# Kernel tuning notes

Measured on AMD Instinct MI355X. Metric: run time of the kernel, lower is better.

Reference implementation:

```python
import jax, jax.numpy as jnp
import numpy as np

N_NODES = 100000
N_EDGES = 1600000
D = 64


def setup_inputs() -> dict:
    key = jax.random.key(0)
    ks = jax.random.split(key, 9)
    x = jax.random.normal(ks[0], (N_NODES, D), dtype=jnp.float32)
    edge_index = jax.random.randint(ks[1], (2, N_EDGES), 0, N_NODES, dtype=jnp.int64)
    W_self = jax.random.normal(ks[2], (D, D), dtype=jnp.float32) * (D ** -0.5)
    b_self = jax.random.normal(ks[3], (D,), dtype=jnp.float32) * 0.01
    W_neigh = jax.random.normal(ks[4], (D, D), dtype=jnp.float32) * (D ** -0.5)
    b_neigh = jax.random.normal(ks[5], (D,), dtype=jnp.float32) * 0.01
    W_var = jax.random.normal(ks[6], (D, D), dtype=jnp.float32) * (D ** -0.5)
    b_var = jax.random.normal(ks[7], (D,), dtype=jnp.float32) * 0.01
    return {"x": x, "edge_index": edge_index, "W_self": W_self, "b_self": b_self,
            "W_neigh": W_neigh, "b_neigh": b_neigh, "W_var": W_var, "b_var": b_var}


def reference(x, edge_index, W_self, b_self, W_neigh, b_neigh, W_var, b_var):
    N, d = x.shape
    scale = d ** -0.5
    src, dst = edge_index[0], edge_index[1]

    x_src = x[src]                                   # [E, d]
    x_dst = x[dst]                                   # [E, d]

    # reciprocal attention: scatter_softmax over incoming edges of dst
    logits = jnp.sum(x_src * x_dst, axis=-1) * scale               # [E]
    seg_max = jax.ops.segment_max(logits, dst, num_segments=N)     # [N]
    ex = jnp.exp(logits - seg_max[dst])                            # [E]
    denom = jax.ops.segment_sum(ex, dst, num_segments=N)           # [N]
    attn = ex / denom[dst]                                         # [E]

    msg = jax.ops.segment_sum(x_src * attn[:, None], dst, num_segments=N)  # [N, d]

    out = x @ W_self.T + b_self + msg @ W_neigh.T + b_neigh

    # variance via double scatter_mean
    cnt = jax.ops.segment_sum(jnp.ones_like(logits), dst, num_segments=N)
    cnt = jnp.maximum(cnt, 1.0)[:, None]                           # [N, 1]
    msg_mean = jax.ops.segment_sum(x_src, dst, num_segments=N) / cnt
    diff_sq = (x_src - msg_mean[dst]) ** 2                         # [E, d]
    var = jax.ops.segment_sum(diff_sq, dst, num_segments=N) / cnt  # [N, d]

    out = out + var @ W_var.T + b_var
    return out
```

## Files before the change

kernel.cpp:

```cpp
#include <hip/hip_runtime.h>


static inline size_t ws_align(size_t x) { return (x + 255) & ~size_t(255); }

typedef __attribute__((ext_vector_type(8))) short bf16x8;
typedef __attribute__((ext_vector_type(4))) float f32x4;
typedef __attribute__((ext_vector_type(2))) float f32x2;

#define ECHUNK 2048

__device__ __forceinline__ unsigned short f2bf(float f) {
    unsigned u = __builtin_bit_cast(unsigned, f);
    u += 0x7FFFu + ((u >> 16) & 1u);
    return (unsigned short)(u >> 16);
}
__device__ __forceinline__ float bfhi(int d) {
    return __builtin_bit_cast(float, (unsigned)d & 0xFFFF0000u);
}
__device__ __forceinline__ float bflo(int d) {
    return __builtin_bit_cast(float, (unsigned)d << 16);
}

template <int CTRL>
__device__ __forceinline__ float dpp_radd(float t) {
    int v = __builtin_amdgcn_update_dpp(0, __builtin_bit_cast(int, t),
                                        CTRL, 0xF, 0xF, true);
    return t + __builtin_bit_cast(float, v);
}
__device__ __forceinline__ float row16_sum(float t) {
    t = dpp_radd<0xB1>(t);
    t = dpp_radd<0x4E>(t);
    t = dpp_radd<0x124>(t);
    t = dpp_radd<0x128>(t);
    return t;
}

__global__ void __launch_bounds__(256) hist_cast_kernel(
        const float* __restrict__ x, unsigned short* __restrict__ xb,
        const int* __restrict__ ei, int* __restrict__ hist,
        int E, int n4, int nblk, int nb1) {
    __shared__ int h[512];
    for (int k = threadIdx.x; k < nb1; k += 256) h[k] = 0;
    int stride = gridDim.x * 256;
    for (int i = blockIdx.x * 256 + threadIdx.x; i < n4; i += stride) {
        float4 v = ((const float4*)x)[i];
        ushort4 hh; hh.x = f2bf(v.x); hh.y = f2bf(v.y); hh.z = f2bf(v.z); hh.w = f2bf(v.w);
        ((ushort4*)xb)[i] = hh;
    }
    __syncthreads();
    const int* dstp = ei + E;
    int base = blockIdx.x * ECHUNK;
    #pragma unroll 4
    for (int k = 0; k < ECHUNK / 256; ++k) {
        int e = base + k * 256 + threadIdx.x;
        if (e < E) atomicAdd(&h[dstp[e] >> 8], 1);
    }
    __syncthreads();
    for (int k = threadIdx.x; k < nb1; k += 256) hist[k * nblk + blockIdx.x] = h[k];
}

__global__ void scan_a_kernel(int* __restrict__ h, int* __restrict__ bsum, int M) {
    __shared__ int t[256];
    int i = blockIdx.x * 256 + threadIdx.x;
    int v = (i < M) ? h[i] : 0;
    t[threadIdx.x] = v;
    __syncthreads();
    for (int off = 1; off < 256; off <<= 1) {
        int u = (threadIdx.x >= (unsigned)off) ? t[threadIdx.x - off] : 0;
        __syncthreads();
        t[threadIdx.x] += u;
        __syncthreads();
    }
    if (i < M) h[i] = t[threadIdx.x] - v;
    if (threadIdx.x == 255) bsum[blockIdx.x] = t[255];
}

__global__ void scan_b_kernel(int* __restrict__ bsum, int nb) {
    __shared__ int t[1024];
    __shared__ int carry;
    if (threadIdx.x == 0) carry = 0;
    __syncthreads();
    for (int base = 0; base < nb; base += 1024) {
        int i = base + threadIdx.x;
        int v = (i < nb) ? bsum[i] : 0;
        t[threadIdx.x] = v;
        __syncthreads();
        for (int off = 1; off < 1024; off <<= 1) {
            int u = (threadIdx.x >= off) ? t[threadIdx.x - off] : 0;
            __syncthreads();
            t[threadIdx.x] += u;
            __syncthreads();
        }
        int c = carry;
        if (i < nb) bsum[i] = t[threadIdx.x] - v + c;
        __syncthreads();
        if (threadIdx.x == 1023) carry = c + t[1023];
        __syncthreads();
    }
}

__global__ void __launch_bounds__(256) part_kernel(
        const int* __restrict__ ei, const int* __restrict__ offs,
        const int* __restrict__ bsum, int* __restrict__ tmp,
        int E, int nblk, int nb1) {
    __shared__ int lofs[512];
    int b = blockIdx.x;
    for (int k = threadIdx.x; k < nb1; k += 256) {
        int idx = k * nblk + b;
        lofs[k] = offs[idx] + bsum[idx >> 8];
    }
    __syncthreads();
    const int* dstp = ei + E;
    int base = b * ECHUNK;
    #pragma unroll 4
    for (int k = 0; k < ECHUNK / 256; ++k) {
        int e = base + k * 256 + threadIdx.x;
        if (e < E) {
            int dst = dstp[e];
            int src = ei[e];
            int pos = atomicAdd(&lofs[dst >> 8], 1);
            tmp[pos] = (src << 8) | (dst & 255);
        }
    }
}

__global__ void __launch_bounds__(256) fsort_kernel(
        const int* __restrict__ tmp, const int* __restrict__ offs,
        const int* __restrict__ bsum, int* __restrict__ srcs,
        int* __restrict__ rs, int E, int N, int nblk, int nb1) {
    __shared__ int cnt[256], sc[256], lofs[256];
    int b = blockIdx.x, tid = threadIdx.x;
    int i0 = b * nblk;
    int start = offs[i0] + bsum[i0 >> 8];
    int end;
    if (b == nb1 - 1) end = E;
    else { int i1 = (b + 1) * nblk; end = offs[i1] + bsum[i1 >> 8]; }

    cnt[tid] = 0;
    __syncthreads();
    for (int e = start + tid; e < end; e += 256) atomicAdd(&cnt[tmp[e] & 255], 1);
    __syncthreads();
    int c = cnt[tid];
    sc[tid] = c;
    __syncthreads();
    for (int off = 1; off < 256; off <<= 1) {
        int u = (tid >= off) ? sc[tid - off] : 0;
        __syncthreads();
        sc[tid] += u;
        __syncthreads();
    }
    int excl = sc[tid] - c;
    int node = b * 256 + tid;
    if (node < N) rs[node] = start + excl;
    lofs[tid] = start + excl;
    __syncthreads();
    for (int e = start + tid; e < end; e += 256) {
        int v = tmp[e];
        int pos = atomicAdd(&lofs[v & 255], 1);
        srcs[pos] = v >> 8;
    }
    if (b == 0 && tid == 0) rs[N] = E;
}

__global__ void __launch_bounds__(256) node_gather_kernel(
        const unsigned short* __restrict__ xb,
        const int* __restrict__ rs, const int* __restrict__ srcs,
        unsigned short* __restrict__ msgvar, int N) {
    int w = (blockIdx.x * blockDim.x + threadIdx.x) >> 6;
    if (w >= N) return;
    int lane = threadIdx.x & 63;
    int q = lane & 15;
    int g = lane >> 4;
    int s = rs[w], e = rs[w + 1];
    const int2* xb2 = (const int2*)xb;
    int2 dn = xb2[(size_t)w * 16 + q];
    f32x2 xn01 = {bflo(dn.x), bfhi(dn.x)}, xn23 = {bflo(dn.y), bfhi(dn.y)};
    float den = 0.f;
    f32x2 sxa = {0,0}, sxb = {0,0}, ssqa = {0,0}, ssqb = {0,0},
          smea = {0,0}, smeb = {0,0};

    auto compute = [&](int2 d) {
        f32x2 a = {bflo(d.x), bfhi(d.x)};
        f32x2 b = {bflo(d.y), bfhi(d.y)};
        f32x2 dp = a * xn01 + b * xn23;
        float t = row16_sum(dp.x + dp.y);
        float ex = __expf(t * 0.125f);
        f32x2 ex2 = {ex, ex};
        den += ex;
        sxa += a;           sxb += b;
        ssqa += a * a;      ssqb += b * b;
        smea += ex2 * a;    smeb += ex2 * b;
    };

    for (int base = s; base < e; base += 64) {
        int cnt = min(e - base, 64);
        int idx = srcs[base + min(lane, cnt - 1)];
        int p = 0;
        int2 da, db;
        if (p + 8 <= cnt) {
            int ra = __shfl(idx, p + g, 64);
            int rb = __shfl(idx, p + 4 + g, 64);
            da = xb2[(size_t)ra * 16 + q];
            db = xb2[(size_t)rb * 16 + q];
        }
        for (; p + 16 <= cnt; p += 8) {
            int ra1 = __shfl(idx, p + 8 + g, 64);
            int rb1 = __shfl(idx, p + 12 + g, 64);
            int2 da1 = xb2[(size_t)ra1 * 16 + q];
            int2 db1 = xb2[(size_t)rb1 * 16 + q];
            compute(da);
            compute(db);
            da = da1; db = db1;
        }
        if (p + 8 <= cnt) {
            compute(da);
            compute(db);
            p += 8;
        }
        if (p + 4 <= cnt) {
            int r = __shfl(idx, p + g, 64);
            compute(xb2[(size_t)r * 16 + q]);
            p += 4;
        }
        if (p < cnt) {
            float wt = (p + g < cnt) ? 1.f : 0.f;
            int r = __shfl(idx, min(p + g, cnt - 1), 64);
            int2 d = xb2[(size_t)r * 16 + q];
            f32x2 a = {bflo(d.x), bfhi(d.x)};
            f32x2 b = {bflo(d.y), bfhi(d.y)};
            f32x2 dp = a * xn01 + b * xn23;
            float t = row16_sum(dp.x + dp.y);
            float ex = __expf(t * 0.125f) * wt;
            f32x2 wt2 = {wt, wt}, ex2 = {ex, ex};
            f32x2 wa = a * wt2, wb = b * wt2;
            den += ex;
            sxa += wa;          sxb += wb;
            ssqa += wa * a;     ssqb += wb * b;
            smea += ex2 * a;    smeb += ex2 * b;
        }
    }
    #pragma unroll
    for (int off = 16; off < 64; off <<= 1) {
        den    += __shfl_xor(den,    off, 64);
        sxa.x  += __shfl_xor(sxa.x,  off, 64); sxa.y  += __shfl_xor(sxa.y,  off, 64);
        sxb.x  += __shfl_xor(sxb.x,  off, 64); sxb.y  += __shfl_xor(sxb.y,  off, 64);
        ssqa.x += __shfl_xor(ssqa.x, off, 64); ssqa.y += __shfl_xor(ssqa.y, off, 64);
        ssqb.x += __shfl_xor(ssqb.x, off, 64); ssqb.y += __shfl_xor(ssqb.y, off, 64);
        smea.x += __shfl_xor(smea.x, off, 64); smea.y += __shfl_xor(smea.y, off, 64);
        smeb.x += __shfl_xor(smeb.x, off, 64); smeb.y += __shfl_xor(smeb.y, off, 64);
    }
    if (lane < 16) {
        float inv = 1.f / fmaxf((float)(e - s), 1.f);
        float invden = (den > 0.f) ? (1.f / den) : 0.f;
        float m0 = sxa.x * inv, m1 = sxa.y * inv, m2 = sxb.x * inv, m3 = sxb.y * inv;
        ushort4 hm, hv;
        hm.x = f2bf(smea.x * invden); hm.y = f2bf(smea.y * invden);
        hm.z = f2bf(smeb.x * invden); hm.w = f2bf(smeb.y * invden);
        hv.x = f2bf(ssqa.x * inv - m0 * m0); hv.y = f2bf(ssqa.y * inv - m1 * m1);
        hv.z = f2bf(ssqb.x * inv - m2 * m2); hv.w = f2bf(ssqb.y * inv - m3 * m3);
        *(ushort4*)&msgvar[(size_t)w * 128 + 4 * q]      = hm;
        *(ushort4*)&msgvar[(size_t)w * 128 + 64 + 4 * q] = hv;
    }
}

__global__ void __launch_bounds__(256) gemm_kernel(
        const unsigned short* __restrict__ xb, const unsigned short* __restrict__ msgvar,
        const float* __restrict__ Ws, const float* __restrict__ bs,
        const float* __restrict__ Wn, const float* __restrict__ bn,
        const float* __restrict__ Wv, const float* __restrict__ bv,
        float* __restrict__ out, int N) {
    __shared__ unsigned short As[64 * 200];
    int tid = threadIdx.x;
    int lane = tid & 63;
    int wv = tid >> 6;
    int j = lane & 15, quad = lane >> 4;
    int jg = wv * 16 + j;

    const float* Wm0[3] = {Ws, Wn, Wv};
    bf16x8 bfrag[6];
    #pragma unroll
    for (int ks = 0; ks < 6; ++ks) {
        const float* W = Wm0[ks >> 1];
        int k0 = (ks & 1) * 32 + quad * 8;
        const float4* p = (const float4*)(W + (size_t)jg * 64 + k0);
        float4 a = p[0], b = p[1];
        bf16x8 f;
        f[0] = (short)f2bf(a.x); f[1] = (short)f2bf(a.y);
        f[2] = (short)f2bf(a.z); f[3] = (short)f2bf(a.w);
        f[4] = (short)f2bf(b.x); f[5] = (short)f2bf(b.y);
        f[6] = (short)f2bf(b.z); f[7] = (short)f2bf(b.w);
        bfrag[ks] = f;
    }
    float bias = bs[jg] + bn[jg] + bv[jg];

    #pragma unroll
    for (int t = 0; t < 2; ++t) {
        int nbase = blockIdx.x * 128 + t * 64;
        #pragma unroll
        for (int i = 0; i < 4; ++i) {
            int idx = i * 256 + tid;
            int row = idx >> 4, c = idx & 15;
            int n = min(nbase + row, N - 1);
            ushort4 h = ((const ushort4*)(xb + (size_t)n * 64))[c];
            *(ushort4*)&As[row * 200 + c * 4] = h;
        }
        #pragma unroll
        for (int i = 0; i < 8; ++i) {
            int idx = i * 256 + tid;
            int row = idx >> 5, c = idx & 31;
            int n = min(nbase + row, N - 1);
            ushort4 h = ((const ushort4*)(msgvar + (size_t)n * 128))[c];
            *(ushort4*)&As[row * 200 + 64 + c * 4] = h;
        }
        __syncthreads();

        f32x4 acc[4];
        #pragma unroll
        for (int nt = 0; nt < 4; ++nt) {
            acc[nt][0] = bias; acc[nt][1] = bias; acc[nt][2] = bias; acc[nt][3] = bias;
        }
        #pragma unroll
        for (int nt = 0; nt < 4; ++nt) {
            #pragma unroll
            for (int ks = 0; ks < 6; ++ks) {
                const bf16x8* ap = (const bf16x8*)&As[(nt * 16 + j) * 200 + ks * 32 + quad * 8];
                acc[nt] = __builtin_amdgcn_mfma_f32_16x16x32_bf16(*ap, bfrag[ks], acc[nt], 0, 0, 0);
            }
        }
        #pragma unroll
        for (int nt = 0; nt < 4; ++nt) {
            #pragma unroll
            for (int r = 0; r < 4; ++r) {
                int node = nbase + nt * 16 + quad * 4 + r;
                if (node < N) out[(size_t)node * 64 + jg] = acc[nt][r];
            }
        }
        __syncthreads();
    }
}

extern "C" void kernel_launch(void* const* d_in, const int* in_sizes, int n_in,
                              void* d_out, int out_size, void* d_ws, size_t ws_size,
                              hipStream_t stream) {
    const float* x  = (const float*)d_in[0];
    const int*   ei = (const int*)d_in[1];
    const float* Ws = (const float*)d_in[2];
    const float* bs = (const float*)d_in[3];
    const float* Wn = (const float*)d_in[4];
    const float* bn = (const float*)d_in[5];
    const float* Wv = (const float*)d_in[6];
    const float* bv = (const float*)d_in[7];
    float* out = (float*)d_out;

    int N  = in_sizes[0] / 64;
    int E  = in_sizes[1] / 2;
    int nblk = (E + ECHUNK - 1) / ECHUNK;
    int nb1  = (N + 255) >> 8;
    int M    = nb1 * nblk;
    int NBs  = (M + 255) / 256;

    char* wsp = (char*)d_ws;
    size_t off = 0;
    int* hist   = (int*)(wsp + off); off += ws_align((size_t)M * 4);
    int* bsumi  = (int*)(wsp + off); off += ws_align((size_t)NBs * 4);
    int* rs     = (int*)(wsp + off); off += ws_align((size_t)(N + 1) * 4);
    int* tmp    = (int*)(wsp + off); off += ws_align((size_t)E * 4);
    int* srcs   = (int*)(wsp + off); off += ws_align((size_t)E * 4);
    unsigned short* msgvar = (unsigned short*)(wsp + off); off += ws_align((size_t)N * 128 * 2);
    unsigned short* xb     = (unsigned short*)(wsp + off); off += ws_align((size_t)N * 64 * 2);

    int n4 = N * 16;
    hist_cast_kernel<<<nblk, 256, 0, stream>>>(x, xb, ei, hist, E, n4, nblk, nb1);
    scan_a_kernel<<<NBs, 256, 0, stream>>>(hist, bsumi, M);
    scan_b_kernel<<<1, 1024, 0, stream>>>(bsumi, NBs);
    part_kernel<<<nblk, 256, 0, stream>>>(ei, hist, bsumi, tmp, E, nblk, nb1);
    fsort_kernel<<<nb1, 256, 0, stream>>>(tmp, hist, bsumi, srcs, rs, E, N, nblk, nb1);
    node_gather_kernel<<<((size_t)N * 64 + 255) / 256, 256, 0, stream>>>(xb, rs, srcs, msgvar, N);
    gemm_kernel<<<(N + 127) / 128, 256, 0, stream>>>(xb, msgvar, Ws, bs, Wn, bn, Wv, bv, out, N);
}
```

Baseline: 207.3 us.

## Enlarge sort chunks, stage fsort segments in LDS, simplify gather tail and reductions

Doubles the edge chunk per block and moves the histogram, partition and fine-sort kernels to 512 threads, which halves the block count and the histogram matrix the scans walk over. The fine-sort kernel now copies its bucket segment into shared memory once when it fits a fixed capacity, so the second pass reads LDS instead of global memory. The gather kernel's tail becomes one masked loop and its cross-group reduction is rewritten through a helper. The changes trade fewer blocks and a larger shared-memory footprint, which can lower occupancy, for less scan and global traffic.

```diff
diff --git a/kernel.cpp b/kernel.cpp
--- a/kernel.cpp
+++ b/kernel.cpp
@@ -7,7 +7,8 @@
 typedef __attribute__((ext_vector_type(4))) float f32x4;
 typedef __attribute__((ext_vector_type(2))) float f32x2;
 
-#define ECHUNK 2048
+#define ECHUNK 4096
+#define FCAP   5120
 
 __device__ __forceinline__ unsigned short f2bf(float f) {
     unsigned u = __builtin_bit_cast(unsigned, f);
@@ -35,14 +36,21 @@
     return t;
 }
 
-__global__ void __launch_bounds__(256) hist_cast_kernel(
+__device__ __forceinline__ float combine4(float t) {
+    t += __shfl_xor(t, 16, 64);
+    t += __shfl_xor(t, 32, 64);
+    return t;
+}
+
+__global__ void __launch_bounds__(512) hist_cast_kernel(
         const float* __restrict__ x, unsigned short* __restrict__ xb,
         const int* __restrict__ ei, int* __restrict__ hist,
         int E, int n4, int nblk, int nb1) {
     __shared__ int h[512];
-    for (int k = threadIdx.x; k < nb1; k += 256) h[k] = 0;
-    int stride = gridDim.x * 256;
-    for (int i = blockIdx.x * 256 + threadIdx.x; i < n4; i += stride) {
+    int tid = threadIdx.x;
+    for (int k = tid; k < nb1; k += 512) h[k] = 0;
+    int stride = gridDim.x * 512;
+    for (int i = blockIdx.x * 512 + tid; i < n4; i += stride) {
         float4 v = ((const float4*)x)[i];
         ushort4 hh; hh.x = f2bf(v.x); hh.y = f2bf(v.y); hh.z = f2bf(v.z); hh.w = f2bf(v.w);
         ((ushort4*)xb)[i] = hh;
@@ -51,12 +59,12 @@
     const int* dstp = ei + E;
     int base = blockIdx.x * ECHUNK;
     #pragma unroll 4
-    for (int k = 0; k < ECHUNK / 256; ++k) {
-        int e = base + k * 256 + threadIdx.x;
+    for (int k = 0; k < ECHUNK / 512; ++k) {
+        int e = base + k * 512 + tid;
         if (e < E) atomicAdd(&h[dstp[e] >> 8], 1);
     }
     __syncthreads();
-    for (int k = threadIdx.x; k < nb1; k += 256) hist[k * nblk + blockIdx.x] = h[k];
+    for (int k = tid; k < nb1; k += 512) hist[k * nblk + blockIdx.x] = h[k];
 }
 
 __global__ void scan_a_kernel(int* __restrict__ h, int* __restrict__ bsum, int M) {
@@ -99,13 +107,13 @@
     }
 }
 
-__global__ void __launch_bounds__(256) part_kernel(
+__global__ void __launch_bounds__(512) part_kernel(
         const int* __restrict__ ei, const int* __restrict__ offs,
         const int* __restrict__ bsum, int* __restrict__ tmp,
         int E, int nblk, int nb1) {
     __shared__ int lofs[512];
-    int b = blockIdx.x;
-    for (int k = threadIdx.x; k < nb1; k += 256) {
+    int b = blockIdx.x, tid = threadIdx.x;
+    for (int k = tid; k < nb1; k += 512) {
         int idx = k * nblk + b;
         lofs[k] = offs[idx] + bsum[idx >> 8];
     }
@@ -113,8 +121,8 @@
     const int* dstp = ei + E;
     int base = b * ECHUNK;
     #pragma unroll 4
-    for (int k = 0; k < ECHUNK / 256; ++k) {
-        int e = base + k * 256 + threadIdx.x;
+    for (int k = 0; k < ECHUNK / 512; ++k) {
+        int e = base + k * 512 + tid;
         if (e < E) {
             int dst = dstp[e];
             int src = ei[e];
@@ -124,40 +132,55 @@
     }
 }
 
-__global__ void __launch_bounds__(256) fsort_kernel(
+__global__ void __launch_bounds__(512) fsort_kernel(
         const int* __restrict__ tmp, const int* __restrict__ offs,
         const int* __restrict__ bsum, int* __restrict__ srcs,
         int* __restrict__ rs, int E, int N, int nblk, int nb1) {
     __shared__ int cnt[256], sc[256], lofs[256];
+    __shared__ int stage[FCAP];
     int b = blockIdx.x, tid = threadIdx.x;
     int i0 = b * nblk;
     int start = offs[i0] + bsum[i0 >> 8];
     int end;
     if (b == nb1 - 1) end = E;
     else { int i1 = (b + 1) * nblk; end = offs[i1] + bsum[i1 >> 8]; }
-
-    cnt[tid] = 0;
-    __syncthreads();
-    for (int e = start + tid; e < end; e += 256) atomicAdd(&cnt[tmp[e] & 255], 1);
-    __syncthreads();
-    int c = cnt[tid];
-    sc[tid] = c;
+    int seg = end - start;
+    bool fit = (seg <= FCAP);
+
+    if (tid < 256) cnt[tid] = 0;
+    if (fit) for (int k = tid; k < seg; k += 512) stage[k] = tmp[start + k];
+    __syncthreads();
+    if (fit) for (int k = tid; k < seg; k += 512) atomicAdd(&cnt[stage[k] & 255], 1);
+    else     for (int e = start + tid; e < end; e += 512) atomicAdd(&cnt[tmp[e] & 255], 1);
+    __syncthreads();
+    int c = (tid < 256) ? cnt[tid] : 0;
+    if (tid < 256) sc[tid] = c;
     __syncthreads();
     for (int off = 1; off < 256; off <<= 1) {
-        int u = (tid >= off) ? sc[tid - off] : 0;
-        __syncthreads();
-        sc[tid] += u;
-        __syncthreads();
-    }
-    int excl = sc[tid] - c;
-    int node = b * 256 + tid;
-    if (node < N) rs[node] = start + excl;
-    lofs[tid] = start + excl;
-    __syncthreads();
-    for (int e = start + tid; e < end; e += 256) {
-        int v = tmp[e];
-        int pos = atomicAdd(&lofs[v & 255], 1);
-        srcs[pos] = v >> 8;
+        int u = (tid < 256 && tid >= off) ? sc[tid - off] : 0;
+        __syncthreads();
+        if (tid < 256) sc[tid] += u;
+        __syncthreads();
+    }
+    if (tid < 256) {
+        int excl = sc[tid] - c;
+        int node = b * 256 + tid;
+        if (node < N) rs[node] = start + excl;
+        lofs[tid] = start + excl;
+    }
+    __syncthreads();
+    if (fit) {
+        for (int k = tid; k < seg; k += 512) {
+            int v = stage[k];
+            int pos = atomicAdd(&lofs[v & 255], 1);
+            srcs[pos] = v >> 8;
+        }
+    } else {
+        for (int e = start + tid; e < end; e += 512) {
+            int v = tmp[e];
+            int pos = atomicAdd(&lofs[v & 255], 1);
+            srcs[pos] = v >> 8;
+        }
     }
     if (b == 0 && tid == 0) rs[N] = E;
 }
@@ -217,12 +240,7 @@
             compute(db);
             p += 8;
         }
-        if (p + 4 <= cnt) {
-            int r = __shfl(idx, p + g, 64);
-            compute(xb2[(size_t)r * 16 + q]);
-            p += 4;
-        }
-        if (p < cnt) {
+        for (; p < cnt; p += 4) {
             float wt = (p + g < cnt) ? 1.f : 0.f;
             int r = __shfl(idx, min(p + g, cnt - 1), 64);
             int2 d = xb2[(size_t)r * 16 + q];
@@ -239,16 +257,13 @@
             smea += ex2 * a;    smeb += ex2 * b;
         }
     }
-    #pragma unroll
-    for (int off = 16; off < 64; off <<= 1) {
-        den    += __shfl_xor(den,    off, 64);
-        sxa.x  += __shfl_xor(sxa.x,  off, 64); sxa.y  += __shfl_xor(sxa.y,  off, 64);
-        sxb.x  += __shfl_xor(sxb.x,  off, 64); sxb.y  += __shfl_xor(sxb.y,  off, 64);
-        ssqa.x += __shfl_xor(ssqa.x, off, 64); ssqa.y += __shfl_xor(ssqa.y, off, 64);
-        ssqb.x += __shfl_xor(ssqb.x, off, 64); ssqb.y += __shfl_xor(ssqb.y, off, 64);
-        smea.x += __shfl_xor(smea.x, off, 64); smea.y += __shfl_xor(smea.y, off, 64);
-        smeb.x += __shfl_xor(smeb.x, off, 64); smeb.y += __shfl_xor(smeb.y, off, 64);
-    }
+    den    = combine4(den);
+    sxa.x  = combine4(sxa.x);  sxa.y  = combine4(sxa.y);
+    sxb.x  = combine4(sxb.x);  sxb.y  = combine4(sxb.y);
+    ssqa.x = combine4(ssqa.x); ssqa.y = combine4(ssqa.y);
+    ssqb.x = combine4(ssqb.x); ssqb.y = combine4(ssqb.y);
+    smea.x = combine4(smea.x); smea.y = combine4(smea.y);
+    smeb.x = combine4(smeb.x); smeb.y = combine4(smeb.y);
     if (lane < 16) {
         float inv = 1.f / fmaxf((float)(e - s), 1.f);
         float invden = (den > 0.f) ? (1.f / den) : 0.f;
@@ -370,11 +385,11 @@
     unsigned short* xb     = (unsigned short*)(wsp + off); off += ws_align((size_t)N * 64 * 2);
 
     int n4 = N * 16;
-    hist_cast_kernel<<<nblk, 256, 0, stream>>>(x, xb, ei, hist, E, n4, nblk, nb1);
+    hist_cast_kernel<<<nblk, 512, 0, stream>>>(x, xb, ei, hist, E, n4, nblk, nb1);
     scan_a_kernel<<<NBs, 256, 0, stream>>>(hist, bsumi, M);
     scan_b_kernel<<<1, 1024, 0, stream>>>(bsumi, NBs);
-    part_kernel<<<nblk, 256, 0, stream>>>(ei, hist, bsumi, tmp, E, nblk, nb1);
-    fsort_kernel<<<nb1, 256, 0, stream>>>(tmp, hist, bsumi, srcs, rs, E, N, nblk, nb1);
+    part_kernel<<<nblk, 512, 0, stream>>>(ei, hist, bsumi, tmp, E, nblk, nb1);
+    fsort_kernel<<<nb1, 512, 0, stream>>>(tmp, hist, bsumi, srcs, rs, E, N, nblk, nb1);
     node_gather_kernel<<<((size_t)N * 64 + 255) / 256, 256, 0, stream>>>(xb, rs, srcs, msgvar, N);
     gemm_kernel<<<(N + 127) / 128, 256, 0, stream>>>(xb, msgvar, Ws, bs, Wn, bn, Wv, bv, out, N);
 }
```

Result: faster. 198.2 us (-4.4%).
